# Kernel optimization log

Measured on AMD Instinct MI355X. Metric: run time of the kernel, lower is better.

Reference implementation:

```python
import jax, jax.numpy as jnp
import numpy as np

B, NL, NP = 8, 256, 16384
DL, DP = 10, 4          # ligand / protein atom-type vocab sizes (one-hot prefix)
L_BIND, L_MREG = 1.0, 0.1
DELTA, EPS, A_C, B_C = 0.01, 1.0, 1.0, 1.0
BOX = 30.0              # Angstrom box for coordinates


def setup_inputs() -> dict:
    key = jax.random.key(0)
    ks = jax.random.split(key, 10)
    return {
        "predicted_noise": jax.random.normal(ks[0], (B, NL, 3), jnp.float32),
        "target_coords": jax.random.normal(ks[1], (B, NL, 3), jnp.float32),
        "scaffold_coords": jax.random.normal(ks[2], (B, NL, 3), jnp.float32),
        "target_coords2": jax.random.uniform(ks[3], (B, NL, 3), jnp.float32) * BOX,
        "target_features": jax.random.uniform(ks[4], (B, NL, DL), jnp.float32),
        "mask": jax.random.uniform(ks[5], (B, NL), jnp.float32),
        "protein_coords": jax.random.uniform(ks[6], (B, NP, 3), jnp.float32) * BOX,
        "protein_features": jax.random.uniform(ks[7], (B, NP, DP), jnp.float32),
        "lig_charge_table": jax.random.normal(ks[8], (DL,), jnp.float32) * 0.3,
        "prot_charge_table": jax.random.normal(ks[9], (DP,), jnp.float32) * 0.3,
    }


def _cdist(x, p):
    # x: [B, NL, 3], p: [B, NP, 3] -> [B, NL, NP] Euclidean distances
    x2 = jnp.sum(x * x, axis=-1)
    p2 = jnp.sum(p * p, axis=-1)
    d2 = x2[:, :, None] + p2[:, None, :] - 2.0 * jnp.einsum('bnd,bmd->bnm', x, p)
    return jnp.sqrt(jnp.maximum(d2, 0.0))


def _binding_energy(x0, prot, lig_feat, prot_feat, lig_tab, prot_tab):
    # atom charges from one-hot prefix of features (argmax lookup)
    ql = lig_tab[jnp.argmax(lig_feat[..., :DL], axis=-1)]    # [B, NL]
    qp = prot_tab[jnp.argmax(prot_feat[..., :DP], axis=-1)]  # [B, NP]
    d = _cdist(x0, prot) + DELTA                             # [B, NL, NP]
    inv = 1.0 / d
    inv6 = inv ** 6
    elec = jnp.sum(ql[:, :, None] * qp[:, None, :] * inv / EPS, axis=(1, 2))
    vdw = jnp.sum(A_C * inv6 * inv6 - B_C * inv6, axis=(1, 2))
    return elec + vdw  # [B]


def reference(predicted_noise, target_coords, scaffold_coords, target_coords2,
              target_features, mask, protein_coords, protein_features,
              lig_charge_table, prot_charge_table):
    msum = jnp.sum(mask)
    # masked denoising MSE
    mse = (predicted_noise - target_coords) ** 2
    loss_denoise = jnp.sum(mse * mask[..., None]) / msum
    # protein-guided binding energy, mean over batch
    loss_bind = jnp.mean(_binding_energy(target_coords2, protein_coords,
                                         target_features, protein_features,
                                         lig_charge_table, prot_charge_table))
    # mask regularization
    mask_diff = jnp.sum((scaffold_coords - target_coords) ** 2, axis=-1)
    loss_mreg = jnp.sum(mask_diff * mask) / msum
    return loss_denoise + L_BIND * loss_bind + L_MREG * loss_mreg
```

## Files before the change

### kernel.cpp

```cpp
#include <hip/hip_runtime.h>
#include <math.h>

#define B   8
#define NL  256
#define NP  16384
#define DL  10
#define DP  4

#define DELTA  0.01f

static __device__ __forceinline__ float fast_sqrtf(float x) {
#if __has_builtin(__builtin_amdgcn_sqrtf)
    return __builtin_amdgcn_sqrtf(x);
#else
    return sqrtf(x);
#endif
}
static __device__ __forceinline__ float fast_rcpf(float x) {
#if __has_builtin(__builtin_amdgcn_rcpf)
    return __builtin_amdgcn_rcpf(x);
#else
    return 1.0f / x;
#endif
}

__global__ __launch_bounds__(256) void prep_kernel(
    const float* __restrict__ prot_coords,
    const float* __restrict__ prot_feat,
    const float* __restrict__ tc2,
    const float* __restrict__ lig_feat,
    const float* __restrict__ lig_tab,
    const float* __restrict__ prot_tab,
    float4* __restrict__ pro4,
    float4* __restrict__ lig4)
{
    if (blockIdx.x < 512) {
        int i = blockIdx.x * 256 + threadIdx.x;
        const float* f = prot_feat + (size_t)i * DP;
        float best = f[0]; int bi = 0;
        #pragma unroll
        for (int j = 1; j < DP; ++j) { float v = f[j]; if (v > best) { best = v; bi = j; } }
        const float* c = prot_coords + (size_t)i * 3;
        pro4[i] = make_float4(c[0], c[1], c[2], prot_tab[bi]);
    } else {
        int i = (blockIdx.x - 512) * 256 + threadIdx.x;
        if (i < B * NL) {
            const float* f = lig_feat + (size_t)i * DL;
            float best = f[0]; int bi = 0;
            #pragma unroll
            for (int j = 1; j < DL; ++j) { float v = f[j]; if (v > best) { best = v; bi = j; } }
            const float* c = tc2 + (size_t)i * 3;
            lig4[i] = make_float4(c[0], c[1], c[2], lig_tab[bi]);
        }
    }
}

__global__ __launch_bounds__(256) void pair_kernel(
    const float4* __restrict__ pro4,
    const float4* __restrict__ lig4,
    double* __restrict__ partials)
{
    const int blk    = blockIdx.x;
    const int lchunk = blk & 3;
    const int pchunk = (blk >> 2) & 63;
    const int b      = blk >> 8;

    const int m = pchunk * 256 + threadIdx.x;
    const float4 p = pro4[b * NP + m];

    const int lbase = b * NL + lchunk * 64;

    float elec = 0.0f, vdw = 0.0f;
    #pragma unroll 4
    for (int j = 0; j < 64; ++j) {
        const float4 l = lig4[lbase + j];
        float dx = l.x - p.x;
        float dy = l.y - p.y;
        float dz = l.z - p.z;
        float d2 = fmaf(dx, dx, fmaf(dy, dy, dz * dz));
        float d  = fast_sqrtf(d2) + DELTA;
        float inv  = fast_rcpf(d);
        float inv2 = inv * inv;
        float inv4 = inv2 * inv2;
        float inv6 = inv4 * inv2;
        elec = fmaf(l.w * p.w, inv, elec);
        vdw  = fmaf(inv6, inv6 - 1.0f, vdw);
    }

    double e = (double)elec, v = (double)vdw;
    #pragma unroll
    for (int off = 32; off > 0; off >>= 1) {
        e += __shfl_down(e, off, 64);
        v += __shfl_down(v, off, 64);
    }
    __shared__ double se[4], sv[4];
    const int lane = threadIdx.x & 63;
    const int w    = threadIdx.x >> 6;
    if (lane == 0) { se[w] = e; sv[w] = v; }
    __syncthreads();
    if (threadIdx.x == 0) {
        partials[2 * blk]     = se[0] + se[1] + se[2] + se[3];
        partials[2 * blk + 1] = sv[0] + sv[1] + sv[2] + sv[3];
    }
}

__global__ __launch_bounds__(256) void finalize_kernel(
    const float*  __restrict__ pred_noise,
    const float*  __restrict__ tgt_coords,
    const float*  __restrict__ scaf_coords,
    const float*  __restrict__ mask,
    const double* __restrict__ partials,
    float* __restrict__ out)
{
    double de = 0.0, mr = 0.0, ms = 0.0, el = 0.0, vd = 0.0;

    for (int i = threadIdx.x; i < B * NL; i += 256) {
        float mk = mask[i];
        float a0 = pred_noise[3*i+0] - tgt_coords[3*i+0];
        float a1 = pred_noise[3*i+1] - tgt_coords[3*i+1];
        float a2 = pred_noise[3*i+2] - tgt_coords[3*i+2];
        de += (double)mk * ((double)a0*a0 + (double)a1*a1 + (double)a2*a2);
        float s0 = scaf_coords[3*i+0] - tgt_coords[3*i+0];
        float s1 = scaf_coords[3*i+1] - tgt_coords[3*i+1];
        float s2 = scaf_coords[3*i+2] - tgt_coords[3*i+2];
        mr += (double)mk * ((double)s0*s0 + (double)s1*s1 + (double)s2*s2);
        ms += (double)mk;
    }
    for (int i = threadIdx.x; i < 2048; i += 256) {
        el += partials[2*i];
        vd += partials[2*i + 1];
    }

    #pragma unroll
    for (int off = 32; off > 0; off >>= 1) {
        de += __shfl_down(de, off, 64);
        mr += __shfl_down(mr, off, 64);
        ms += __shfl_down(ms, off, 64);
        el += __shfl_down(el, off, 64);
        vd += __shfl_down(vd, off, 64);
    }
    __shared__ double s[4][5];
    const int lane = threadIdx.x & 63;
    const int w    = threadIdx.x >> 6;
    if (lane == 0) { s[w][0]=de; s[w][1]=mr; s[w][2]=ms; s[w][3]=el; s[w][4]=vd; }
    __syncthreads();
    if (threadIdx.x == 0) {
        de = s[0][0]+s[1][0]+s[2][0]+s[3][0];
        mr = s[0][1]+s[1][1]+s[2][1]+s[3][1];
        ms = s[0][2]+s[1][2]+s[2][2]+s[3][2];
        el = s[0][3]+s[1][3]+s[2][3]+s[3][3];
        vd = s[0][4]+s[1][4]+s[2][4]+s[3][4];
        double loss_bind = (el + vd) / (double)B;
        double loss = de / ms + 1.0 * loss_bind + 0.1 * (mr / ms);
        out[0] = (float)loss;
    }
}

extern "C" void kernel_launch(void* const* d_in, const int* in_sizes, int n_in,
                              void* d_out, int out_size, void* d_ws, size_t ws_size,
                              hipStream_t stream)
{
    const float* pred_noise  = (const float*)d_in[0];
    const float* tgt_coords  = (const float*)d_in[1];
    const float* scaf_coords = (const float*)d_in[2];
    const float* tc2         = (const float*)d_in[3];
    const float* lig_feat    = (const float*)d_in[4];
    const float* mask        = (const float*)d_in[5];
    const float* prot_coords = (const float*)d_in[6];
    const float* prot_feat   = (const float*)d_in[7];
    const float* lig_tab     = (const float*)d_in[8];
    const float* prot_tab    = (const float*)d_in[9];
    float* out = (float*)d_out;

    char* ws = (char*)d_ws;
    float4* pro4     = (float4*)ws;
    float4* lig4     = (float4*)(ws + (size_t)B * NP * sizeof(float4));
    double* partials = (double*)(ws + (size_t)B * NP * sizeof(float4)
                                    + (size_t)B * NL * sizeof(float4));

    prep_kernel<<<520, 256, 0, stream>>>(prot_coords, prot_feat, tc2, lig_feat,
                                         lig_tab, prot_tab, pro4, lig4);
    pair_kernel<<<2048, 256, 0, stream>>>(pro4, lig4, partials);
    finalize_kernel<<<1, 256, 0, stream>>>(pred_noise, tgt_coords, scaf_coords,
                                           mask, partials, out);
}
```

Baseline: 101.8 us.

## Fuse prep into pair kernel and move masked MSE into extra blocks

Removes the separate prep kernel: each pair block now computes its ligand charges and coordinates into shared memory and its protein charge inline, so there is no workspace round trip and one fewer launch. The per-pair charge product is hoisted so the protein charge multiplies the accumulated elec sum once. The denoise and regularisation sums move from the single-block finalize into 8 extra blocks of the main kernel. In exchange, argmax work is repeated across the blocks that share the same data, and a block barrier is added before the pair loop.

```diff
diff --git a/kernel.cpp b/kernel.cpp
--- a/kernel.cpp
+++ b/kernel.cpp
@@ -24,134 +24,155 @@
 #endif
 }
 
-__global__ __launch_bounds__(256) void prep_kernel(
+#define NBIND 2048
+#define NMSE  8
+
+__global__ __launch_bounds__(256) void pair_mse_kernel(
     const float* __restrict__ prot_coords,
     const float* __restrict__ prot_feat,
     const float* __restrict__ tc2,
     const float* __restrict__ lig_feat,
     const float* __restrict__ lig_tab,
     const float* __restrict__ prot_tab,
-    float4* __restrict__ pro4,
-    float4* __restrict__ lig4)
-{
-    if (blockIdx.x < 512) {
-        int i = blockIdx.x * 256 + threadIdx.x;
-        const float* f = prot_feat + (size_t)i * DP;
-        float best = f[0]; int bi = 0;
-        #pragma unroll
-        for (int j = 1; j < DP; ++j) { float v = f[j]; if (v > best) { best = v; bi = j; } }
-        const float* c = prot_coords + (size_t)i * 3;
-        pro4[i] = make_float4(c[0], c[1], c[2], prot_tab[bi]);
-    } else {
-        int i = (blockIdx.x - 512) * 256 + threadIdx.x;
-        if (i < B * NL) {
-            const float* f = lig_feat + (size_t)i * DL;
-            float best = f[0]; int bi = 0;
-            #pragma unroll
-            for (int j = 1; j < DL; ++j) { float v = f[j]; if (v > best) { best = v; bi = j; } }
-            const float* c = tc2 + (size_t)i * 3;
-            lig4[i] = make_float4(c[0], c[1], c[2], lig_tab[bi]);
-        }
-    }
-}
-
-__global__ __launch_bounds__(256) void pair_kernel(
-    const float4* __restrict__ pro4,
-    const float4* __restrict__ lig4,
+    const float* __restrict__ pred_noise,
+    const float* __restrict__ tgt_coords,
+    const float* __restrict__ scaf_coords,
+    const float* __restrict__ mask,
     double* __restrict__ partials)
 {
-    const int blk    = blockIdx.x;
-    const int lchunk = blk & 3;
-    const int pchunk = (blk >> 2) & 63;
-    const int b      = blk >> 8;
-
-    const int m = pchunk * 256 + threadIdx.x;
-    const float4 p = pro4[b * NP + m];
-
-    const int lbase = b * NL + lchunk * 64;
-
-    float elec = 0.0f, vdw = 0.0f;
-    #pragma unroll 4
-    for (int j = 0; j < 64; ++j) {
-        const float4 l = lig4[lbase + j];
-        float dx = l.x - p.x;
-        float dy = l.y - p.y;
-        float dz = l.z - p.z;
-        float d2 = fmaf(dx, dx, fmaf(dy, dy, dz * dz));
-        float d  = fast_sqrtf(d2) + DELTA;
-        float inv  = fast_rcpf(d);
-        float inv2 = inv * inv;
-        float inv4 = inv2 * inv2;
-        float inv6 = inv4 * inv2;
-        elec = fmaf(l.w * p.w, inv, elec);
-        vdw  = fmaf(inv6, inv6 - 1.0f, vdw);
-    }
-
-    double e = (double)elec, v = (double)vdw;
-    #pragma unroll
-    for (int off = 32; off > 0; off >>= 1) {
-        e += __shfl_down(e, off, 64);
-        v += __shfl_down(v, off, 64);
-    }
-    __shared__ double se[4], sv[4];
-    const int lane = threadIdx.x & 63;
-    const int w    = threadIdx.x >> 6;
-    if (lane == 0) { se[w] = e; sv[w] = v; }
-    __syncthreads();
-    if (threadIdx.x == 0) {
-        partials[2 * blk]     = se[0] + se[1] + se[2] + se[3];
-        partials[2 * blk + 1] = sv[0] + sv[1] + sv[2] + sv[3];
-    }
-}
-
-__global__ __launch_bounds__(256) void finalize_kernel(
-    const float*  __restrict__ pred_noise,
-    const float*  __restrict__ tgt_coords,
-    const float*  __restrict__ scaf_coords,
-    const float*  __restrict__ mask,
-    const double* __restrict__ partials,
-    float* __restrict__ out)
-{
-    double de = 0.0, mr = 0.0, ms = 0.0, el = 0.0, vd = 0.0;
-
-    for (int i = threadIdx.x; i < B * NL; i += 256) {
+    const int tid = threadIdx.x;
+    const int blk = blockIdx.x;
+
+    if (blk < NBIND) {
+        const int lchunk = blk & 3;
+        const int pchunk = (blk >> 2) & 63;
+        const int b      = blk >> 8;
+
+        __shared__ float4 slig[64];
+        if (tid < 64) {
+            const int li = b * NL + lchunk * 64 + tid;
+            const float* f = lig_feat + (size_t)li * DL;
+            float best = f[0]; float q = lig_tab[0];
+            #pragma unroll
+            for (int j = 1; j < DL; ++j) {
+                float v = f[j];
+                float t = lig_tab[j];
+                if (v > best) { best = v; q = t; }
+            }
+            const float* c = tc2 + (size_t)li * 3;
+            slig[tid] = make_float4(c[0], c[1], c[2], q);
+        }
+
+        const int m = b * NP + pchunk * 256 + tid;
+        const float* pc = prot_coords + (size_t)m * 3;
+        const float px = pc[0], py = pc[1], pz = pc[2];
+        const float4 pf = reinterpret_cast<const float4*>(prot_feat)[m];
+        float qb = pf.x, qp = prot_tab[0];
+        { float t = prot_tab[1]; if (pf.y > qb) { qb = pf.y; qp = t; } }
+        { float t = prot_tab[2]; if (pf.z > qb) { qb = pf.z; qp = t; } }
+        { float t = prot_tab[3]; if (pf.w > qb) { qb = pf.w; qp = t; } }
+
+        __syncthreads();
+
+        float eacc = 0.0f, vacc = 0.0f;
+        #pragma unroll 8
+        for (int j = 0; j < 64; ++j) {
+            const float4 l = slig[j];
+            float dx = l.x - px;
+            float dy = l.y - py;
+            float dz = l.z - pz;
+            float d2 = fmaf(dx, dx, fmaf(dy, dy, dz * dz));
+            float d  = fast_sqrtf(d2) + DELTA;
+            float inv  = fast_rcpf(d);
+            float inv2 = inv * inv;
+            float inv6 = inv2 * inv2 * inv2;
+            eacc = fmaf(l.w, inv, eacc);
+            vacc = fmaf(inv6, inv6 - 1.0f, vacc);
+        }
+        double e = (double)(qp * eacc);
+        double v = (double)vacc;
+
+        #pragma unroll
+        for (int off = 32; off > 0; off >>= 1) {
+            e += __shfl_down(e, off, 64);
+            v += __shfl_down(v, off, 64);
+        }
+        __shared__ double se[4], sv[4];
+        const int lane = tid & 63, w = tid >> 6;
+        if (lane == 0) { se[w] = e; sv[w] = v; }
+        __syncthreads();
+        if (tid == 0) {
+            partials[2 * blk]     = se[0] + se[1] + se[2] + se[3];
+            partials[2 * blk + 1] = sv[0] + sv[1] + sv[2] + sv[3];
+        }
+    } else {
+        const int idx = blk - NBIND;
+        const int i   = idx * 256 + tid;
         float mk = mask[i];
         float a0 = pred_noise[3*i+0] - tgt_coords[3*i+0];
         float a1 = pred_noise[3*i+1] - tgt_coords[3*i+1];
         float a2 = pred_noise[3*i+2] - tgt_coords[3*i+2];
-        de += (double)mk * ((double)a0*a0 + (double)a1*a1 + (double)a2*a2);
+        double de = (double)mk * ((double)a0*a0 + (double)a1*a1 + (double)a2*a2);
         float s0 = scaf_coords[3*i+0] - tgt_coords[3*i+0];
         float s1 = scaf_coords[3*i+1] - tgt_coords[3*i+1];
         float s2 = scaf_coords[3*i+2] - tgt_coords[3*i+2];
-        mr += (double)mk * ((double)s0*s0 + (double)s1*s1 + (double)s2*s2);
-        ms += (double)mk;
-    }
-    for (int i = threadIdx.x; i < 2048; i += 256) {
+        double mr = (double)mk * ((double)s0*s0 + (double)s1*s1 + (double)s2*s2);
+        double ms = (double)mk;
+
+        #pragma unroll
+        for (int off = 32; off > 0; off >>= 1) {
+            de += __shfl_down(de, off, 64);
+            mr += __shfl_down(mr, off, 64);
+            ms += __shfl_down(ms, off, 64);
+        }
+        __shared__ double s[4][3];
+        const int lane = tid & 63, w = tid >> 6;
+        if (lane == 0) { s[w][0] = de; s[w][1] = mr; s[w][2] = ms; }
+        __syncthreads();
+        if (tid == 0) {
+            partials[2*NBIND + idx*3 + 0] = s[0][0]+s[1][0]+s[2][0]+s[3][0];
+            partials[2*NBIND + idx*3 + 1] = s[0][1]+s[1][1]+s[2][1]+s[3][1];
+            partials[2*NBIND + idx*3 + 2] = s[0][2]+s[1][2]+s[2][2]+s[3][2];
+        }
+    }
+}
+
+__global__ __launch_bounds__(256) void finalize_kernel(
+    const double* __restrict__ partials,
+    float* __restrict__ out)
+{
+    const int tid = threadIdx.x;
+    double el = 0.0, vd = 0.0;
+    for (int i = tid; i < NBIND; i += 256) {
         el += partials[2*i];
         vd += partials[2*i + 1];
     }
-
+    double de = 0.0, mr = 0.0, ms = 0.0;
+    if (tid < NMSE) {
+        de = partials[2*NBIND + tid*3 + 0];
+        mr = partials[2*NBIND + tid*3 + 1];
+        ms = partials[2*NBIND + tid*3 + 2];
+    }
     #pragma unroll
     for (int off = 32; off > 0; off >>= 1) {
+        el += __shfl_down(el, off, 64);
+        vd += __shfl_down(vd, off, 64);
         de += __shfl_down(de, off, 64);
         mr += __shfl_down(mr, off, 64);
         ms += __shfl_down(ms, off, 64);
-        el += __shfl_down(el, off, 64);
-        vd += __shfl_down(vd, off, 64);
     }
     __shared__ double s[4][5];
-    const int lane = threadIdx.x & 63;
-    const int w    = threadIdx.x >> 6;
-    if (lane == 0) { s[w][0]=de; s[w][1]=mr; s[w][2]=ms; s[w][3]=el; s[w][4]=vd; }
+    const int lane = tid & 63, w = tid >> 6;
+    if (lane == 0) { s[w][0]=el; s[w][1]=vd; s[w][2]=de; s[w][3]=mr; s[w][4]=ms; }
     __syncthreads();
-    if (threadIdx.x == 0) {
-        de = s[0][0]+s[1][0]+s[2][0]+s[3][0];
-        mr = s[0][1]+s[1][1]+s[2][1]+s[3][1];
-        ms = s[0][2]+s[1][2]+s[2][2]+s[3][2];
-        el = s[0][3]+s[1][3]+s[2][3]+s[3][3];
-        vd = s[0][4]+s[1][4]+s[2][4]+s[3][4];
+    if (tid == 0) {
+        el = s[0][0]+s[1][0]+s[2][0]+s[3][0];
+        vd = s[0][1]+s[1][1]+s[2][1]+s[3][1];
+        de = s[0][2]+s[1][2]+s[2][2]+s[3][2];
+        mr = s[0][3]+s[1][3]+s[2][3]+s[3][3];
+        ms = s[0][4]+s[1][4]+s[2][4]+s[3][4];
         double loss_bind = (el + vd) / (double)B;
-        double loss = de / ms + 1.0 * loss_bind + 0.1 * (mr / ms);
+        double loss = de / ms + loss_bind + 0.1 * (mr / ms);
         out[0] = (float)loss;
     }
 }
@@ -172,15 +193,10 @@
     const float* prot_tab    = (const float*)d_in[9];
     float* out = (float*)d_out;
 
-    char* ws = (char*)d_ws;
-    float4* pro4     = (float4*)ws;
-    float4* lig4     = (float4*)(ws + (size_t)B * NP * sizeof(float4));
-    double* partials = (double*)(ws + (size_t)B * NP * sizeof(float4)
-                                    + (size_t)B * NL * sizeof(float4));
-
-    prep_kernel<<<520, 256, 0, stream>>>(prot_coords, prot_feat, tc2, lig_feat,
-                                         lig_tab, prot_tab, pro4, lig4);
-    pair_kernel<<<2048, 256, 0, stream>>>(pro4, lig4, partials);
-    finalize_kernel<<<1, 256, 0, stream>>>(pred_noise, tgt_coords, scaf_coords,
-                                           mask, partials, out);
-}
+    double* partials = (double*)d_ws;
+
+    pair_mse_kernel<<<NBIND + NMSE, 256, 0, stream>>>(
+        prot_coords, prot_feat, tc2, lig_feat, lig_tab, prot_tab,
+        pred_noise, tgt_coords, scaf_coords, mask, partials);
+    finalize_kernel<<<1, 256, 0, stream>>>(partials, out);
+}
```

New measurement: 94.97 us. 1.07x faster.
